# Optimization experiments

Measured on AMD Instinct MI355X. Metric: run time of the kernel, lower is better.

## Reference

```python
import jax, jax.numpy as jnp
import numpy as np

B, T, C = 2, 2048, 2048
H, KV = 16, 4
D = C // H            # 128 head dim
G = H // KV           # 4 query heads per kv head
THETA = 10000.0


def setup_inputs() -> dict:
    key = jax.random.key(0)
    k0, k1, k2, k3 = jax.random.split(key, 4)
    s = 1.0 / np.sqrt(C)
    return {
        "x": jax.random.normal(k0, (B, T, C), jnp.float32),
        "Wq": jax.random.normal(k1, (H * D, C), jnp.float32) * s,
        "Wkv": jax.random.normal(k2, (2 * KV * D, C), jnp.float32) * s,
        "Wo": jax.random.normal(k3, (C, C), jnp.float32) * s,
    }


def _rotate_half(x):
    d = x.shape[-1] // 2
    return jnp.concatenate([-x[..., d:], x[..., :d]], axis=-1)


def _rope_tables(t, d):
    freqs = 1.0 / (THETA ** (jnp.arange(0, d, 2, dtype=jnp.float32) / d))
    ang = jnp.arange(t, dtype=jnp.float32)[:, None] * freqs[None, :]  # [T, d/2]
    emb = jnp.concatenate([ang, ang], axis=-1)                         # [T, d]
    return jnp.cos(emb), jnp.sin(emb)


def reference(x, Wq, Wkv, Wo):
    b, t, c = x.shape
    q = (x @ Wq.T).reshape(b, t, H, D).transpose(0, 2, 1, 3)      # [B,H,T,D]
    kv = (x @ Wkv.T).reshape(b, t, 2 * KV, D)
    k = kv[:, :, :KV].transpose(0, 2, 1, 3)                        # [B,KV,T,D]
    v = kv[:, :, KV:].transpose(0, 2, 1, 3)                        # [B,KV,T,D]

    cos, sin = _rope_tables(t, D)
    cos, sin = cos[None, None], sin[None, None]                    # [1,1,T,D]
    q = q * cos + _rotate_half(q) * sin
    k = k * cos + _rotate_half(k) * sin

    # GQA: keep k/v at KV heads; reshape q into [B,KV,G,T,D] instead of expanding k/v.
    qg = q.reshape(b, KV, G, t, D)
    scores = jnp.einsum('bkgtd,bksd->bkgts', qg, k) / jnp.sqrt(jnp.float32(D))
    causal = jnp.tril(jnp.ones((t, t), dtype=bool))                # is_causal=True path
    scores = jnp.where(causal, scores, -jnp.inf)
    p = jax.nn.softmax(scores, axis=-1)
    y = jnp.einsum('bkgts,bksd->bkgtd', p, v)                      # [B,KV,G,T,D]
    y = y.reshape(b, H, t, D).transpose(0, 2, 1, 3).reshape(b, t, c)
    return y @ Wo.T
```

## Files before the change

kernel.cpp:

```cpp
#include <hip/hip_runtime.h>

typedef unsigned short u16;
typedef __attribute__((ext_vector_type(4))) float f32x4;
typedef __attribute__((ext_vector_type(16))) float f32x16;
typedef __attribute__((ext_vector_type(8))) __bf16 bf16x8;

__device__ __forceinline__ u16 f2bf(float f) {
    unsigned int x = __float_as_uint(f);
    x += 0x7fffu + ((x >> 16) & 1u);
    return (u16)(x >> 16);
}
__device__ __forceinline__ float bf2f(u16 u) {
    return __uint_as_float(((unsigned int)u) << 16);
}
__device__ __forceinline__ void async16(const void* g, void* l) {
    __builtin_amdgcn_global_load_lds(
        (const __attribute__((address_space(1))) void*)g,
        (__attribute__((address_space(3))) void*)l,
        16, 0, 0);
}
__device__ __forceinline__ void barrier_fence() {
    asm volatile("" ::: "memory");
    __builtin_amdgcn_s_barrier();
    asm volatile("" ::: "memory");
}
__device__ __forceinline__ unsigned cvtpk(float lo, float hi) {
    unsigned d;
    asm("v_cvt_pk_bf16_f32 %0, %1, %2" : "=v"(d) : "v"(lo), "v"(hi));
    return d;
}

__global__ __launch_bounds__(256)
void cvt_all(const float* __restrict__ x,  const float* __restrict__ wq,
             const float* __restrict__ wkv, const float* __restrict__ wo,
             u16* __restrict__ xb, u16* __restrict__ wqb,
             u16* __restrict__ wkvb, u16* __restrict__ wob)
{
    const int nx = 8388608, nq = 4194304, nkv = 2097152;
    const int i = (blockIdx.x * 256 + threadIdx.x) * 4;
    const float* src; u16* dst; int off;
    if (i < nx)                 { src = x;   dst = xb;   off = i; }
    else if (i < nx + nq)       { src = wq;  dst = wqb;  off = i - nx; }
    else if (i < nx + nq + nkv) { src = wkv; dst = wkvb; off = i - nx - nq; }
    else                        { src = wo;  dst = wob;  off = i - nx - nq - nkv; }
    const float4 v = *(const float4*)(src + off);
    ushort4 o;
    o.x = f2bf(v.x); o.y = f2bf(v.y); o.z = f2bf(v.z); o.w = f2bf(v.w);
    *(ushort4*)(dst + off) = o;
}

__global__ __launch_bounds__(256, 3)
void gemm_qkv(const u16* __restrict__ A,
              const u16* __restrict__ B0,
              const u16* __restrict__ B1,
              u16* __restrict__ C,
              u16* __restrict__ vbuf,
              int M, int K)
{
    constexpr int ASZ = 128 * 32;
    __shared__ __align__(16) u16 As[3 * ASZ];
    __shared__ __align__(16) u16 Bs[3 * ASZ];

    const int tid  = threadIdx.x;
    const int w    = tid >> 6;
    const int lane = tid & 63;
    const int fl   = lane & 15;
    const int q4   = lane >> 4;
    const int wm   = w >> 1;
    const int wn   = w & 1;

    const int gx  = gridDim.x;
    const int nwg = gx * gridDim.y;
    int id = blockIdx.y * gx + blockIdx.x;
    id = (id & 7) * (nwg >> 3) + (id >> 3);
    const int m0 = (id / gx) * 128;
    const int n0 = (id % gx) * 128;

    const u16* Bp = B0;
    int nb = n0;
    if (n0 >= 2048) { Bp = B1; nb = n0 - 2048; }

    const int srow = w * 16 + (lane >> 2);
    const int sg   = (lane & 3) ^ ((lane >> 3) & 3);
    const u16* agp = A  + (size_t)(m0 + srow) * K + sg * 8;
    const u16* bgp = Bp + (size_t)(nb + srow) * K + sg * 8;
    const int sLds = w * 512;

    const int cSlot = (q4 ^ ((fl >> 1) & 3)) * 8;

    f32x4 acc[4][4];
    #pragma unroll
    for (int i = 0; i < 4; ++i)
        #pragma unroll
        for (int j = 0; j < 4; ++j)
            acc[i][j] = f32x4{0.f, 0.f, 0.f, 0.f};

    const int NT = K >> 5;

    auto stage = [&](int t, int bf) {
        const size_t kof = (size_t)t * 32;
        async16(agp + kof,                   &As[bf * ASZ + sLds]);
        async16(agp + (size_t)64 * K + kof,  &As[bf * ASZ + 2048 + sLds]);
        async16(bgp + kof,                   &Bs[bf * ASZ + sLds]);
        async16(bgp + (size_t)64 * K + kof,  &Bs[bf * ASZ + 2048 + sLds]);
    };

    stage(0, 0);
    stage(1, 1);

    int bf = 0;
    for (int t = 0; t < NT; ++t) {
        if (t < NT - 1) asm volatile("s_waitcnt vmcnt(4)" ::: "memory");
        else            asm volatile("s_waitcnt vmcnt(0)" ::: "memory");
        barrier_fence();
        const int bf2 = (bf + 2 >= 3) ? bf - 1 : bf + 2;
        if (t + 2 < NT) stage(t + 2, bf2);

        const int ab = bf * ASZ + (wm * 64 + fl) * 32 + cSlot;
        const int bb = bf * ASZ + (wn * 32 + fl) * 32 + cSlot;
        bf16x8 a[4], b[4];
        #pragma unroll
        for (int mt = 0; mt < 4; ++mt)
            a[mt] = *(const bf16x8*)&As[ab + mt * 512];
        b[0] = *(const bf16x8*)&Bs[bb];
        b[1] = *(const bf16x8*)&Bs[bb + 512];
        b[2] = *(const bf16x8*)&Bs[bb + 2048];
        b[3] = *(const bf16x8*)&Bs[bb + 2560];

        #pragma unroll
        for (int mt = 0; mt < 4; ++mt)
            #pragma unroll
            for (int nt = 0; nt < 4; ++nt)
                acc[mt][nt] = __builtin_amdgcn_mfma_f32_16x16x32_bf16(
                    a[mt], b[nt], acc[mt][nt], 0, 0, 0);

        bf = (bf + 1 >= 3) ? 0 : bf + 1;
    }

    if (n0 < 2560) {
        const float sc = (n0 < 2048) ? 0.08838834764831845f : 1.0f;
        float inv[2];
        #pragma unroll
        for (int j = 0; j < 2; ++j)
            inv[j] = exp2f(-(float)(wn * 32 + j * 16 + fl) * 0.2076205f);
        #pragma unroll
        for (int mt = 0; mt < 4; ++mt) {
            #pragma unroll
            for (int r = 0; r < 4; ++r) {
                const int row = m0 + wm * 64 + mt * 16 + q4 * 4 + r;
                const float pos = (float)(row & 2047);
                #pragma unroll
                for (int j = 0; j < 2; ++j) {
                    float s, c;
                    __sincosf(pos * inv[j], &s, &c);
                    const float x1 = acc[mt][j][r];
                    const float x2 = acc[mt][j + 2][r];
                    const int i0 = wn * 32 + j * 16 + fl;
                    C[(size_t)row * 3072 + n0 + i0]      = f2bf((x1 * c - x2 * s) * sc);
                    C[(size_t)row * 3072 + n0 + 64 + i0] = f2bf((x2 * c + x1 * s) * sc);
                }
            }
        }
    } else {
        #pragma unroll
        for (int mt = 0; mt < 4; ++mt)
            #pragma unroll
            for (int j = 0; j < 4; ++j) {
                const int colb = n0 + wn * 32 + (j & 1) * 16 + (j >> 1) * 64 + fl;
                const int f = colb - 2560;
                #pragma unroll
                for (int r = 0; r < 4; ++r) {
                    const int row = m0 + wm * 64 + mt * 16 + q4 * 4 + r;
                    const int tt = row & 2047;
                    const int bb2 = row >> 11;
                    vbuf[((size_t)((bb2 << 2) + (f >> 7)) * 128 + (f & 127)) * 2048 + tt] =
                        f2bf(acc[mt][j][r]);
                }
            }
    }
}

__global__ __launch_bounds__(256, 3)
void gemm128r(const u16* __restrict__ A,
              const u16* __restrict__ B0,
              float* __restrict__ Cf,
              int M, int N, int K)
{
    constexpr int ASZ = 128 * 32;
    __shared__ __align__(16) u16 As[3 * ASZ];
    __shared__ __align__(16) u16 Bs[3 * ASZ];

    const int tid  = threadIdx.x;
    const int w    = tid >> 6;
    const int lane = tid & 63;
    const int fl   = lane & 15;
    const int q4   = lane >> 4;
    const int wm   = w >> 1;
    const int wn   = w & 1;

    const int gx  = gridDim.x;
    const int nwg = gx * gridDim.y;
    int id = blockIdx.y * gx + blockIdx.x;
    id = (id & 7) * (nwg >> 3) + (id >> 3);
    const int m0 = (id / gx) * 128;
    const int n0 = (id % gx) * 128;

    const int srow = w * 16 + (lane >> 2);
    const int sg   = (lane & 3) ^ ((lane >> 3) & 3);
    const u16* agp = A  + (size_t)(m0 + srow) * K + sg * 8;
    const u16* bgp = B0 + (size_t)(n0 + srow) * K + sg * 8;
    const int sLds = w * 512;

    const int cSlot = (q4 ^ ((fl >> 1) & 3)) * 8;

    f32x4 acc[4][4];
    #pragma unroll
    for (int i = 0; i < 4; ++i)
        #pragma unroll
        for (int j = 0; j < 4; ++j)
            acc[i][j] = f32x4{0.f, 0.f, 0.f, 0.f};

    const int NT = K >> 5;

    auto stage = [&](int t, int bf) {
        const size_t kof = (size_t)t * 32;
        async16(agp + kof,                   &As[bf * ASZ + sLds]);
        async16(agp + (size_t)64 * K + kof,  &As[bf * ASZ + 2048 + sLds]);
        async16(bgp + kof,                   &Bs[bf * ASZ + sLds]);
        async16(bgp + (size_t)64 * K + kof,  &Bs[bf * ASZ + 2048 + sLds]);
    };

    stage(0, 0);
    stage(1, 1);

    int bf = 0;
    for (int t = 0; t < NT; ++t) {
        if (t < NT - 1) asm volatile("s_waitcnt vmcnt(4)" ::: "memory");
        else            asm volatile("s_waitcnt vmcnt(0)" ::: "memory");
        barrier_fence();
        const int bf2 = (bf + 2 >= 3) ? bf - 1 : bf + 2;
        if (t + 2 < NT) stage(t + 2, bf2);

        const int ab = bf * ASZ + (wm * 64 + fl) * 32 + cSlot;
        const int bb = bf * ASZ + (wn * 64 + fl) * 32 + cSlot;
        bf16x8 a[4], b[4];
        #pragma unroll
        for (int mt = 0; mt < 4; ++mt)
            a[mt] = *(const bf16x8*)&As[ab + mt * 512];
        #pragma unroll
        for (int nt = 0; nt < 4; ++nt)
            b[nt] = *(const bf16x8*)&Bs[bb + nt * 512];

        #pragma unroll
        for (int mt = 0; mt < 4; ++mt)
            #pragma unroll
            for (int nt = 0; nt < 4; ++nt)
                acc[mt][nt] = __builtin_amdgcn_mfma_f32_16x16x32_bf16(
                    a[mt], b[nt], acc[mt][nt], 0, 0, 0);

        bf = (bf + 1 >= 3) ? 0 : bf + 1;
    }

    #pragma unroll
    for (int mt = 0; mt < 4; ++mt)
        #pragma unroll
        for (int nt = 0; nt < 4; ++nt) {
            const int colb = n0 + wn * 64 + nt * 16 + fl;
            #pragma unroll
            for (int r = 0; r < 4; ++r) {
                const int row = m0 + wm * 64 + mt * 16 + q4 * 4 + r;
                Cf[(size_t)row * N + colb] = acc[mt][nt][r];
            }
        }
}

__global__ __launch_bounds__(256, 2)
void attn_kernel(const u16* __restrict__ qkv,
                 const u16* __restrict__ vsrc,
                 u16* __restrict__ y)
{
    constexpr int T = 2048;
    const int bh = blockIdx.x;
    const int by = blockIdx.y;
    const int qt = (by < 8) ? by : 23 - by;
    const int b = bh >> 4, h = bh & 15, kvh = h >> 2;

    const int tid  = threadIdx.x;
    const int w    = tid >> 6;
    const int lane = tid & 63;
    const int l31  = lane & 31;
    const int hh   = lane >> 5;

    __shared__ __align__(16) u16 Ks[2][32 * 128];
    __shared__ __align__(16) u16 Vt[2][128 * 32];

    const u16* Qg = qkv  + (size_t)(b * T) * 3072 + (h << 7);
    const u16* Kg = qkv  + (size_t)(b * T) * 3072 + 2048 + (kvh << 7);
    const u16* Vg = vsrc + (size_t)((b * 4 + kvh) * 128) * T;

    const int qb = qt * 128 + w * 32;
    bf16x8 qf[8];
    #pragma unroll
    for (int kc = 0; kc < 8; ++kc)
        qf[kc] = *(const bf16x8*)&Qg[(size_t)(qb + l31) * 3072 + kc * 16 + hh * 8];

    int goffK[2], goffV[2], ldsC[2];
    #pragma unroll
    for (int i = 0; i < 2; ++i) {
        const int c  = w + 4 * i;
        const int rk = 4 * c + (lane >> 4);
        const int lk = (lane & 15) ^ (rk & 15);
        goffK[i] = rk * 3072 + lk * 8;
        const int rv = 16 * c + (lane >> 2);
        const int lv = (lane & 3) ^ ((lane >> 3) & 3);
        goffV[i] = rv * T + lv * 8;
        ldsC[i]  = c * 512;
    }

    #pragma unroll
    for (int i = 0; i < 2; ++i) {
        async16(Kg + goffK[i], &Ks[0][ldsC[i]]);
        async16(Vg + goffV[i], &Vt[0][ldsC[i]]);
    }

    f32x16 o[4];
    #pragma unroll
    for (int dt = 0; dt < 4; ++dt)
        #pragma unroll
        for (int r = 0; r < 16; ++r)
            o[dt][r] = 0.f;
    float lsum = 0.f;

    const int NJ = 4 * qt + 4;
    const int jw = 4 * qt + w;
    const int aswz = l31 & 15;
    const int vswz = (l31 >> 1) & 3;

    for (int j = 0; j < NJ; ++j) {
        __syncthreads();

        if (j + 1 < NJ) {
            const u16* kb = Kg + (size_t)(j + 1) * 32 * 3072;
            const u16* vb = Vg + (j + 1) * 32;
            const int nb = (j + 1) & 1;
            #pragma unroll
            for (int i = 0; i < 2; ++i) {
                async16(kb + goffK[i], &Ks[nb][ldsC[i]]);
                async16(vb + goffV[i], &Vt[nb][ldsC[i]]);
            }
        }
        const int cb = j & 1;
        if (j > jw) continue;

        f32x16 s;
        #pragma unroll
        for (int r = 0; r < 16; ++r) s[r] = 0.f;
        #pragma unroll
        for (int kc = 0; kc < 8; ++kc) {
            bf16x8 aK = *(const bf16x8*)
                &Ks[cb][l31 * 128 + ((2 * kc + hh) ^ aswz) * 8];
            s = __builtin_amdgcn_mfma_f32_32x32x16_bf16(aK, qf[kc], s, 0, 0, 0);
        }

        if (j == jw) {
            #pragma unroll
            for (int r = 0; r < 16; ++r) {
                const int kvl = (r & 3) + 8 * (r >> 2) + 4 * hh;
                if (kvl > l31) s[r] = -3e38f;
            }
        }

        float p[16];
        #pragma unroll
        for (int r = 0; r < 16; ++r) {
            p[r] = __expf(s[r]);
            lsum += p[r];
        }

        #pragma unroll
        for (int kc = 0; kc < 2; ++kc) {
            unsigned A0 = cvtpk(p[8 * kc + 0], p[8 * kc + 1]);
            unsigned A1 = cvtpk(p[8 * kc + 2], p[8 * kc + 3]);
            unsigned B0 = cvtpk(p[8 * kc + 4], p[8 * kc + 5]);
            unsigned B1 = cvtpk(p[8 * kc + 6], p[8 * kc + 7]);
            asm volatile("v_permlane32_swap_b32 %0, %1" : "+v"(A0), "+v"(B0));
            asm volatile("v_permlane32_swap_b32 %0, %1" : "+v"(A1), "+v"(B1));
            union { unsigned u[4]; bf16x8 v; } pu;
            pu.u[0] = A0; pu.u[1] = A1; pu.u[2] = B0; pu.u[3] = B1;
            const bf16x8 pa = pu.v;
            #pragma unroll
            for (int dt = 0; dt < 4; ++dt) {
                bf16x8 bv = *(const bf16x8*)
                    &Vt[cb][(dt * 32 + l31) * 32 + ((2 * kc + hh) ^ vswz) * 8];
                o[dt] = __builtin_amdgcn_mfma_f32_32x32x16_bf16(pa, bv, o[dt], 0, 0, 0);
            }
        }
    }

    lsum += __shfl_xor(lsum, 32, 64);
    const float linv = 1.0f / lsum;

    #pragma unroll
    for (int r = 0; r < 16; ++r) {
        const int qloc = (r & 3) + 8 * (r >> 2) + 4 * hh;
        const float lr = __shfl(linv, qloc, 64);
        const size_t row = (size_t)(b * T + qb + qloc);
        #pragma unroll
        for (int dt = 0; dt < 4; ++dt)
            y[row * 2048 + (h << 7) + dt * 32 + l31] = f2bf(o[dt][r] * lr);
    }
}

extern "C" void kernel_launch(void* const* d_in, const int* in_sizes, int n_in,
                              void* d_out, int out_size, void* d_ws, size_t ws_size,
                              hipStream_t stream)
{
    const float* x   = (const float*)d_in[0];
    const float* Wq  = (const float*)d_in[1];
    const float* Wkv = (const float*)d_in[2];
    const float* Wo  = (const float*)d_in[3];
    float* out = (float*)d_out;

    const int nx = 4096 * 2048, nq = 2048 * 2048, nkv = 1024 * 2048, no = 2048 * 2048;

    u16* xb   = (u16*)d_ws;
    u16* wqb  = xb  + nx;
    u16* wkvb = wqb + nq;
    u16* wob  = wkvb + nkv;
    u16* qkv  = wob + no;
    u16* vbuf = qkv + (size_t)4096 * 3072;
    u16* y    = vbuf + (size_t)2 * 4 * 128 * 2048;

    const int ntot = nx + nq + nkv + no;
    cvt_all<<<ntot / 1024, 256, 0, stream>>>(x, Wq, Wkv, Wo, xb, wqb, wkvb, wob);

    dim3 g1(3072 / 128, 4096 / 128);
    gemm_qkv<<<g1, 256, 0, stream>>>(xb, wqb, wkvb, qkv, vbuf, 4096, 2048);

    attn_kernel<<<dim3(32, 16), 256, 0, stream>>>(qkv, vbuf, y);

    dim3 g2(2048 / 128, 4096 / 128);
    gemm128r<<<g2, 256, 0, stream>>>(y, wob, out, 4096, 2048, 2048);
}
```

Before: 289.5 us.

## Pair low and high causal query tiles per attention block sharing K/V

Each attention block now handles two query tiles, one near the start of the sequence and its mirror near the end, so every block does the same amount of causal work. Each K/V tile loaded into LDS is reused by both tiles. The grid shrinks to 256 blocks (one per CU), and block ids are remapped so heads that share a KV head sit next to each other. Staging becomes a three-buffer pipeline with explicit vmcnt waits, which keeps two tiles in flight. The cost is roughly double the accumulator registers and launch bounds dropped to one block per CU, which lowers occupancy and latency hiding.

```diff
diff --git a/kernel.cpp b/kernel.cpp
--- a/kernel.cpp
+++ b/kernel.cpp
@@ -28,6 +28,17 @@
     unsigned d;
     asm("v_cvt_pk_bf16_f32 %0, %1, %2" : "=v"(d) : "v"(lo), "v"(hi));
     return d;
+}
+__device__ __forceinline__ bf16x8 build_pa(const float* p) {
+    unsigned A0 = cvtpk(p[0], p[1]);
+    unsigned A1 = cvtpk(p[2], p[3]);
+    unsigned B0 = cvtpk(p[4], p[5]);
+    unsigned B1 = cvtpk(p[6], p[7]);
+    asm volatile("v_permlane32_swap_b32 %0, %1" : "+v"(A0), "+v"(B0));
+    asm volatile("v_permlane32_swap_b32 %0, %1" : "+v"(A1), "+v"(B1));
+    union { unsigned u[4]; bf16x8 v; } pu;
+    pu.u[0] = A0; pu.u[1] = A1; pu.u[2] = B0; pu.u[3] = B1;
+    return pu.v;
 }
 
 __global__ __launch_bounds__(256)
@@ -274,16 +285,19 @@
         }
 }
 
-__global__ __launch_bounds__(256, 2)
+__global__ __launch_bounds__(256, 1)
 void attn_kernel(const u16* __restrict__ qkv,
                  const u16* __restrict__ vsrc,
                  u16* __restrict__ y)
 {
     constexpr int T = 2048;
-    const int bh = blockIdx.x;
-    const int by = blockIdx.y;
-    const int qt = (by < 8) ? by : 23 - by;
-    const int b = bh >> 4, h = bh & 15, kvh = h >> 2;
+    const int id  = blockIdx.x;
+    const int p   = id & 7;
+    const int bh  = p * 4 + ((id >> 3) & 3);
+    const int lp  = id >> 5;
+    const int lo  = lp;
+    const int hi  = 15 - lp;
+    const int b   = bh >> 4, h = bh & 15, kvh = h >> 2;
 
     const int tid  = threadIdx.x;
     const int w    = tid >> 6;
@@ -291,18 +305,21 @@
     const int l31  = lane & 31;
     const int hh   = lane >> 5;
 
-    __shared__ __align__(16) u16 Ks[2][32 * 128];
-    __shared__ __align__(16) u16 Vt[2][128 * 32];
+    __shared__ __align__(16) u16 Ks[3][32 * 128];
+    __shared__ __align__(16) u16 Vt[3][128 * 32];
 
     const u16* Qg = qkv  + (size_t)(b * T) * 3072 + (h << 7);
     const u16* Kg = qkv  + (size_t)(b * T) * 3072 + 2048 + (kvh << 7);
     const u16* Vg = vsrc + (size_t)((b * 4 + kvh) * 128) * T;
 
-    const int qb = qt * 128 + w * 32;
-    bf16x8 qf[8];
-    #pragma unroll
-    for (int kc = 0; kc < 8; ++kc)
-        qf[kc] = *(const bf16x8*)&Qg[(size_t)(qb + l31) * 3072 + kc * 16 + hh * 8];
+    const int q0 = lo * 128 + w * 32;
+    const int q1 = hi * 128 + w * 32;
+    bf16x8 qf0[8], qf1[8];
+    #pragma unroll
+    for (int kc = 0; kc < 8; ++kc) {
+        qf0[kc] = *(const bf16x8*)&Qg[(size_t)(q0 + l31) * 3072 + kc * 16 + hh * 8];
+        qf1[kc] = *(const bf16x8*)&Qg[(size_t)(q1 + l31) * 3072 + kc * 16 + hh * 8];
+    }
 
     int goffK[2], goffV[2], ldsC[2];
     #pragma unroll
@@ -317,97 +334,113 @@
         ldsC[i]  = c * 512;
     }
 
-    #pragma unroll
-    for (int i = 0; i < 2; ++i) {
-        async16(Kg + goffK[i], &Ks[0][ldsC[i]]);
-        async16(Vg + goffV[i], &Vt[0][ldsC[i]]);
-    }
-
-    f32x16 o[4];
+    auto stage = [&](int t, int bf) {
+        const u16* kb = Kg + (size_t)t * 32 * 3072;
+        const u16* vb = Vg + t * 32;
+        #pragma unroll
+        for (int i = 0; i < 2; ++i) {
+            async16(kb + goffK[i], &Ks[bf][ldsC[i]]);
+            async16(vb + goffV[i], &Vt[bf][ldsC[i]]);
+        }
+    };
+
+    f32x16 o0[4], o1[4];
     #pragma unroll
     for (int dt = 0; dt < 4; ++dt)
         #pragma unroll
-        for (int r = 0; r < 16; ++r)
-            o[dt][r] = 0.f;
-    float lsum = 0.f;
-
-    const int NJ = 4 * qt + 4;
-    const int jw = 4 * qt + w;
+        for (int r = 0; r < 16; ++r) { o0[dt][r] = 0.f; o1[dt][r] = 0.f; }
+    float ls0 = 0.f, ls1 = 0.f;
+
+    const int NJ  = 4 * hi + 4;
+    const int jw0 = 4 * lo + w;
+    const int jw1 = 4 * hi + w;
     const int aswz = l31 & 15;
     const int vswz = (l31 >> 1) & 3;
 
+    stage(0, 0);
+    stage(1, 1);
+    int bf = 0;
     for (int j = 0; j < NJ; ++j) {
-        __syncthreads();
-
-        if (j + 1 < NJ) {
-            const u16* kb = Kg + (size_t)(j + 1) * 32 * 3072;
-            const u16* vb = Vg + (j + 1) * 32;
-            const int nb = (j + 1) & 1;
-            #pragma unroll
-            for (int i = 0; i < 2; ++i) {
-                async16(kb + goffK[i], &Ks[nb][ldsC[i]]);
-                async16(vb + goffV[i], &Vt[nb][ldsC[i]]);
-            }
+        if (j < NJ - 1) asm volatile("s_waitcnt vmcnt(4)" ::: "memory");
+        else            asm volatile("s_waitcnt vmcnt(0)" ::: "memory");
+        barrier_fence();
+        const int bf2 = (bf + 2 >= 3) ? bf - 1 : bf + 2;
+        if (j + 2 < NJ) stage(j + 2, bf2);
+
+        const bool a0 = (j <= jw0);
+        const bool a1 = (j <= jw1);
+        if (a0 || a1) {
+            f32x16 s0, s1;
+            #pragma unroll
+            for (int r = 0; r < 16; ++r) { s0[r] = 0.f; s1[r] = 0.f; }
+            #pragma unroll
+            for (int kc = 0; kc < 8; ++kc) {
+                bf16x8 aK = *(const bf16x8*)
+                    &Ks[bf][l31 * 128 + ((2 * kc + hh) ^ aswz) * 8];
+                if (a1) s1 = __builtin_amdgcn_mfma_f32_32x32x16_bf16(aK, qf1[kc], s1, 0, 0, 0);
+                if (a0) s0 = __builtin_amdgcn_mfma_f32_32x32x16_bf16(aK, qf0[kc], s0, 0, 0, 0);
+            }
+            if (j == jw1) {
+                #pragma unroll
+                for (int r = 0; r < 16; ++r) {
+                    const int kvl = (r & 3) + 8 * (r >> 2) + 4 * hh;
+                    if (kvl > l31) s1[r] = -3e38f;
+                }
+            }
+            if (j == jw0) {
+                #pragma unroll
+                for (int r = 0; r < 16; ++r) {
+                    const int kvl = (r & 3) + 8 * (r >> 2) + 4 * hh;
+                    if (kvl > l31) s0[r] = -3e38f;
+                }
+            }
+
+            bf16x8 pA0[2], pA1[2];
+            if (a1) {
+                float pr[16];
+                #pragma unroll
+                for (int r = 0; r < 16; ++r) { pr[r] = __expf(s1[r]); ls1 += pr[r]; }
+                pA1[0] = build_pa(&pr[0]);
+                pA1[1] = build_pa(&pr[8]);
+            }
+            if (a0) {
+                float pr[16];
+                #pragma unroll
+                for (int r = 0; r < 16; ++r) { pr[r] = __expf(s0[r]); ls0 += pr[r]; }
+                pA0[0] = build_pa(&pr[0]);
+                pA0[1] = build_pa(&pr[8]);
+            }
+
+            #pragma unroll
+            for (int kc = 0; kc < 2; ++kc)
+                #pragma unroll
+                for (int dt = 0; dt < 4; ++dt) {
+                    bf16x8 bv = *(const bf16x8*)
+                        &Vt[bf][(dt * 32 + l31) * 32 + ((2 * kc + hh) ^ vswz) * 8];
+                    if (a1) o1[dt] = __builtin_amdgcn_mfma_f32_32x32x16_bf16(pA1[kc], bv, o1[dt], 0, 0, 0);
+                    if (a0) o0[dt] = __builtin_amdgcn_mfma_f32_32x32x16_bf16(pA0[kc], bv, o0[dt], 0, 0, 0);
+                }
         }
-        const int cb = j & 1;
-        if (j > jw) continue;
-
-        f32x16 s;
-        #pragma unroll
-        for (int r = 0; r < 16; ++r) s[r] = 0.f;
-        #pragma unroll
-        for (int kc = 0; kc < 8; ++kc) {
-            bf16x8 aK = *(const bf16x8*)
-                &Ks[cb][l31 * 128 + ((2 * kc + hh) ^ aswz) * 8];
-            s = __builtin_amdgcn_mfma_f32_32x32x16_bf16(aK, qf[kc], s, 0, 0, 0);
-        }
-
-        if (j == jw) {
-            #pragma unroll
-            for (int r = 0; r < 16; ++r) {
-                const int kvl = (r & 3) + 8 * (r >> 2) + 4 * hh;
-                if (kvl > l31) s[r] = -3e38f;
-            }
-        }
-
-        float p[16];
-        #pragma unroll
-        for (int r = 0; r < 16; ++r) {
-            p[r] = __expf(s[r]);
-            lsum += p[r];
-        }
-
-        #pragma unroll
-        for (int kc = 0; kc < 2; ++kc) {
-            unsigned A0 = cvtpk(p[8 * kc + 0], p[8 * kc + 1]);
-            unsigned A1 = cvtpk(p[8 * kc + 2], p[8 * kc + 3]);
-            unsigned B0 = cvtpk(p[8 * kc + 4], p[8 * kc + 5]);
-            unsigned B1 = cvtpk(p[8 * kc + 6], p[8 * kc + 7]);
-            asm volatile("v_permlane32_swap_b32 %0, %1" : "+v"(A0), "+v"(B0));
-            asm volatile("v_permlane32_swap_b32 %0, %1" : "+v"(A1), "+v"(B1));
-            union { unsigned u[4]; bf16x8 v; } pu;
-            pu.u[0] = A0; pu.u[1] = A1; pu.u[2] = B0; pu.u[3] = B1;
-            const bf16x8 pa = pu.v;
-            #pragma unroll
-            for (int dt = 0; dt < 4; ++dt) {
-                bf16x8 bv = *(const bf16x8*)
-                    &Vt[cb][(dt * 32 + l31) * 32 + ((2 * kc + hh) ^ vswz) * 8];
-                o[dt] = __builtin_amdgcn_mfma_f32_32x32x16_bf16(pa, bv, o[dt], 0, 0, 0);
-            }
-        }
-    }
-
-    lsum += __shfl_xor(lsum, 32, 64);
-    const float linv = 1.0f / lsum;
+        bf = (bf + 1 >= 3) ? 0 : bf + 1;
+    }
+
+    ls0 += __shfl_xor(ls0, 32, 64);
+    ls1 += __shfl_xor(ls1, 32, 64);
+    const float li0 = 1.0f / ls0;
+    const float li1 = 1.0f / ls1;
 
     #pragma unroll
     for (int r = 0; r < 16; ++r) {
         const int qloc = (r & 3) + 8 * (r >> 2) + 4 * hh;
-        const float lr = __shfl(linv, qloc, 64);
-        const size_t row = (size_t)(b * T + qb + qloc);
-        #pragma unroll
-        for (int dt = 0; dt < 4; ++dt)
-            y[row * 2048 + (h << 7) + dt * 32 + l31] = f2bf(o[dt][r] * lr);
+        const float lr0 = __shfl(li0, qloc, 64);
+        const float lr1 = __shfl(li1, qloc, 64);
+        const size_t row0 = (size_t)(b * T + q0 + qloc);
+        const size_t row1 = (size_t)(b * T + q1 + qloc);
+        #pragma unroll
+        for (int dt = 0; dt < 4; ++dt) {
+            y[row0 * 2048 + (h << 7) + dt * 32 + l31] = f2bf(o0[dt][r] * lr0);
+            y[row1 * 2048 + (h << 7) + dt * 32 + l31] = f2bf(o1[dt][r] * lr1);
+        }
     }
 }
 
@@ -437,7 +470,7 @@
     dim3 g1(3072 / 128, 4096 / 128);
     gemm_qkv<<<g1, 256, 0, stream>>>(xb, wqb, wkvb, qkv, vbuf, 4096, 2048);
 
-    attn_kernel<<<dim3(32, 16), 256, 0, stream>>>(qkv, vbuf, y);
+    attn_kernel<<<256, 256, 0, stream>>>(qkv, vbuf, y);
 
     dim3 g2(2048 / 128, 4096 / 128);
     gemm128r<<<g2, 256, 0, stream>>>(y, wob, out, 4096, 2048, 2048);
```

Result: slower. 337.1 us (+16.4%).
